# Optimization experiments

Hardware: AMD Instinct MI355X
Metric: run time of the kernel (lower is better)

Reference implementation:

```python
import jax, jax.numpy as jnp
import numpy as np

N, E, G, R = 65536, 524288, 1024, 512
D_IN, H, R_FEAT, NH, HD = 7, 128, 25, 4, 32
EPS = 1e-5


def setup_inputs() -> dict:
    key = jax.random.key(0)
    ks = jax.random.split(key, 16)
    f = lambda i, shape, s: jax.random.normal(ks[i], shape, jnp.float32) * s
    return {
        "x": jax.random.normal(ks[0], (N, D_IN), jnp.float32),
        "edge_index": jax.random.randint(ks[1], (2, E), 0, N),
        "batch": jnp.repeat(jnp.arange(G), N // G),  # 64 atoms per graph, sorted
        "per_residue_features": jax.random.normal(ks[2], (R, R_FEAT), jnp.float32),
        # GCN layer weights (PyG GCNConv: x @ W then normalized aggregation, + bias)
        "W0": f(3, (D_IN, H), 0.3), "b0": jnp.zeros(H, jnp.float32),
        "W1": f(4, (H, H), 0.1), "b1": jnp.zeros(H, jnp.float32),
        "W2": f(5, (H, H), 0.1), "b2": jnp.zeros(H, jnp.float32),
        # BatchNorm (eval mode, running stats)
        "bn_gamma": jnp.ones((3, H), jnp.float32),
        "bn_beta": jnp.zeros((3, H), jnp.float32),
        "bn_mean": f(6, (3, H), 0.1),
        "bn_var": jax.random.uniform(ks[7], (3, H), jnp.float32) + 0.5,
        # residue projection
        "res_W": f(8, (R_FEAT, H), 0.2), "res_b": jnp.zeros(H, jnp.float32),
        # MultiheadAttention packed in-proj (rows: q, k, v) and out-proj
        "in_W": f(9, (3 * H, H), 0.08), "in_b": jnp.zeros(3 * H, jnp.float32),
        "out_W": f(10, (H, H), 0.08), "out_b": jnp.zeros(H, jnp.float32),
        # classifier 128 -> 64 -> 1
        "cls_W1": f(11, (H, 64), 0.1), "cls_b1": jnp.zeros(64, jnp.float32),
        "cls_W2": f(12, (64, 1), 0.1), "cls_b2": jnp.zeros(1, jnp.float32),
    }


def reference(x, edge_index, batch, per_residue_features,
              W0, b0, W1, b1, W2, b2,
              bn_gamma, bn_beta, bn_mean, bn_var,
              res_W, res_b, in_W, in_b, out_W, out_b,
              cls_W1, cls_b1, cls_W2, cls_b2):
    src, dst = edge_index[0], edge_index[1]
    # GCN symmetric norm with self-loops: deg[i] = 1 + in-degree(i)
    deg = jnp.ones(N, x.dtype).at[dst].add(1.0)
    dinv = jax.lax.rsqrt(deg)
    enorm = (dinv[src] * dinv[dst])[:, None]      # [E,1]
    self_norm = (dinv * dinv)[:, None]            # [N,1]

    def gcn_bn_relu(h, W, b, i):
        m = h @ W                                  # [N,H]
        agg = m * self_norm
        agg = agg.at[dst].add(m[src] * enorm) + b
        y = bn_gamma[i] * (agg - bn_mean[i]) * jax.lax.rsqrt(bn_var[i] + EPS) + bn_beta[i]
        return jax.nn.relu(y)  # dropout is identity at inference

    h = gcn_bn_relu(x, W0, b0, 0)
    h = gcn_bn_relu(h, W1, b1, 1)
    h = gcn_bn_relu(h, W2, b2, 2)

    # shared residue KV (same for every graph) -> fused attention over all nodes
    res = per_residue_features @ res_W + res_b     # [R,H]
    Wq, Wk, Wv = jnp.split(in_W, 3, axis=0)
    bq, bk, bv = jnp.split(in_b, 3)
    q = (h @ Wq.T + bq).reshape(N, NH, HD)
    k = (res @ Wk.T + bk).reshape(R, NH, HD)
    v = (res @ Wv.T + bv).reshape(R, NH, HD)
    scores = jnp.einsum('nhd,rhd->nhr', q, k) / np.float32(np.sqrt(HD))
    attn = jax.nn.softmax(scores, axis=-1)         # [N,NH,R]
    o = jnp.einsum('nhr,rhd->nhd', attn, v).reshape(N, H)
    o = o @ out_W.T + out_b                        # [N,H]

    # per-graph mean pool (segment mean over batch ids)
    counts = jnp.zeros(G, o.dtype).at[batch].add(1.0)
    pooled = jnp.zeros((G, H), o.dtype).at[batch].add(o) / counts[:, None]

    hid = jax.nn.relu(pooled @ cls_W1 + cls_b1)
    logits = (hid @ cls_W2 + cls_b2)[:, 0]         # [G]
    return logits
```

## Files before the change

### kernel.cpp

```cpp
#include <hip/hip_runtime.h>
#include <math.h>

#define N_NODES 65536
#define N_EDGES 524288
#define N_GRAPHS 1024
#define H 128
#define R_RES 512
#define NH 4
#define HD 32
#define D_IN 7
#define EPS 1e-5f

typedef __attribute__((ext_vector_type(8))) short short8;
typedef __attribute__((ext_vector_type(4))) short short4v;
typedef __attribute__((ext_vector_type(4))) float f32x4;
typedef __attribute__((ext_vector_type(4))) unsigned uint4v;
typedef __attribute__((ext_vector_type(2))) unsigned uint2v;
typedef __attribute__((ext_vector_type(4))) unsigned short us4;

#if __has_builtin(__builtin_amdgcn_exp2f)
#define EXP2F __builtin_amdgcn_exp2f
#else
#define EXP2F exp2f
#endif
#if __has_builtin(__builtin_amdgcn_rcpf)
#define RCPF __builtin_amdgcn_rcpf
#else
#define RCPF(x) (1.0f/(x))
#endif

__device__ __forceinline__ f32x4 mfma_k16(short4v a, short4v b, f32x4 c){
#if defined(__HIP_DEVICE_COMPILE__)
  return __builtin_amdgcn_mfma_f32_16x16x16bf16_1k(a, b, c, 0, 0, 0);
#else
  (void)a; (void)b; return c;
#endif
}

__device__ __forceinline__ unsigned short rnd_bf16(float f){
  return (unsigned short)((__builtin_bit_cast(unsigned, f) + 0x8000u) >> 16);
}
__device__ __forceinline__ unsigned pk_bf16(float lo, float hi){
  unsigned a = __builtin_bit_cast(unsigned, lo) + 0x8000u;
  unsigned b = __builtin_bit_cast(unsigned, hi) + 0x8000u;
  return __builtin_amdgcn_perm(b, a, 0x07060302u);
}
__device__ __forceinline__ float bflo(unsigned u){ return __builtin_bit_cast(float, u << 16); }
__device__ __forceinline__ float bfhi(unsigned u){ return __builtin_bit_cast(float, u & 0xFFFF0000u); }

__device__ __forceinline__ void acc8(float* a, uint4v u, float wgt){
  a[0]=fmaf(bflo(u.x),wgt,a[0]); a[1]=fmaf(bfhi(u.x),wgt,a[1]);
  a[2]=fmaf(bflo(u.y),wgt,a[2]); a[3]=fmaf(bfhi(u.y),wgt,a[3]);
  a[4]=fmaf(bflo(u.z),wgt,a[4]); a[5]=fmaf(bfhi(u.z),wgt,a[5]);
  a[6]=fmaf(bflo(u.w),wgt,a[6]); a[7]=fmaf(bfhi(u.w),wgt,a[7]);
}

__global__ __launch_bounds__(256) void k_count(const int* __restrict__ dst, int* __restrict__ cnt, int E){
  int e = blockIdx.x*256 + threadIdx.x;
  if (e < E) atomicAdd(&cnt[dst[e]], 1);
}

__global__ __launch_bounds__(256) void k_part(const int* __restrict__ cnt, int* __restrict__ part){
  int i = blockIdx.x*256 + threadIdx.x;
  int v = cnt[i];
  #pragma unroll
  for (int off=1; off<64; off<<=1) v += __shfl_xor(v, off);
  __shared__ int red[4];
  if ((threadIdx.x & 63) == 0) red[threadIdx.x >> 6] = v;
  __syncthreads();
  if (threadIdx.x == 0) part[blockIdx.x] = red[0]+red[1]+red[2]+red[3];
}

__global__ __launch_bounds__(256) void k_scanp(int* __restrict__ part){
  __shared__ int s[256];
  int t = threadIdx.x;
  int v = part[t];
  s[t] = v;
  __syncthreads();
  for (int off=1; off<256; off<<=1){
    int u = (t >= off) ? s[t-off] : 0;
    __syncthreads();
    s[t] += u;
    __syncthreads();
  }
  part[t] = s[t] - v;
}

__global__ __launch_bounds__(256) void k_apply(const int* __restrict__ cnt, const int* __restrict__ part,
      int* __restrict__ csr_off, int* __restrict__ cursor, float* __restrict__ dinv){
  __shared__ int s[256];
  int b = blockIdx.x, t = threadIdx.x;
  int i = b*256 + t;
  int c = cnt[i];
  s[t] = c;
  __syncthreads();
  for (int off=1; off<256; off<<=1){
    int u = (t >= off) ? s[t-off] : 0;
    __syncthreads();
    s[t] += u;
    __syncthreads();
  }
  int o0 = part[b] + s[t] - c;
  csr_off[i] = o0;
  cursor[i] = o0;
  dinv[i] = rsqrtf(1.0f + (float)c);
  if (i == N_NODES-1) csr_off[N_NODES] = N_EDGES;
}

__global__ __launch_bounds__(256) void k_fill(const int* __restrict__ src, const int* __restrict__ dst,
      const float* __restrict__ dinv, int* __restrict__ cursor, int2* __restrict__ csr_ev, int E){
  int e = blockIdx.x*256 + threadIdx.x;
  if (e >= E) return;
  int s = src[e], d = dst[e];
  int p = atomicAdd(&cursor[d], 1);
  int2 rec;
  rec.x = s;
  rec.y = __builtin_bit_cast(int, dinv[s]*dinv[d]);
  csr_ev[p] = rec;
}

__global__ __launch_bounds__(256) void k_lin0(const float* __restrict__ x, const float* __restrict__ W0,
                                              unsigned short* __restrict__ out){
  int gid = blockIdx.x*256 + threadIdx.x;
  int l = threadIdx.x & 63;
  int n = __builtin_amdgcn_readfirstlane(gid >> 6);
  float a0 = 0.0f, a1 = 0.0f;
  #pragma unroll
  for (int k=0;k<D_IN;k++){
    float xv = x[(long)n*D_IN + k];
    float2 wv = *(const float2*)(W0 + k*H + 2*l);
    a0 = fmaf(xv, wv.x, a0); a1 = fmaf(xv, wv.y, a1);
  }
  *(unsigned*)(out + (long)n*H + 2*l) = pk_bf16(a0, a1);
}

__global__ __launch_bounds__(256) void k_gemm_mfma(const unsigned short* __restrict__ A,
      const float* __restrict__ Bsrc, const float* __restrict__ bias, void* __restrict__ Cout,
      int transB, int outMode){
  __shared__ unsigned short Bt[128][136];
  int tid = threadIdx.x;
  long rowBase = (long)blockIdx.x * 128;
  int w = tid >> 6, l = tid & 63;
  int lc = l & 15, q4 = l >> 4;

  if (transB){
    for (int i = tid; i < 4096; i += 256){
      int c = i >> 5, seg = i & 31;
      float4 v = *(const float4*)(Bsrc + (long)c*128 + seg*4);
      uint2 p; p.x = pk_bf16(v.x, v.y); p.y = pk_bf16(v.z, v.w);
      *(uint2*)&Bt[c][seg*4] = p;
    }
  } else {
    for (int i = tid; i < 4096; i += 256){
      int k = i >> 5, seg = i & 31;
      float4 v = *(const float4*)(Bsrc + (long)k*128 + seg*4);
      Bt[seg*4+0][k] = rnd_bf16(v.x); Bt[seg*4+1][k] = rnd_bf16(v.y);
      Bt[seg*4+2][k] = rnd_bf16(v.z); Bt[seg*4+3][k] = rnd_bf16(v.w);
    }
  }

  short8 af[2][4];
  #pragma unroll
  for (int rt=0;rt<2;rt++){
    long row = rowBase + w*32 + rt*16 + lc;
    #pragma unroll
    for (int kc=0;kc<4;kc++)
      af[rt][kc] = *(const short8*)(A + row*128 + kc*32 + q4*8);
  }

  f32x4 acc[2][8];
  #pragma unroll
  for (int rt=0;rt<2;rt++)
    #pragma unroll
    for (int ct=0;ct<8;ct++) acc[rt][ct] = (f32x4){0.f,0.f,0.f,0.f};

  __syncthreads();

  #pragma unroll
  for (int kc=0;kc<4;kc++){
    #pragma unroll
    for (int ct=0;ct<8;ct++){
      short8 bf = *(const short8*)&Bt[ct*16 + lc][kc*32 + q4*8];
      acc[0][ct] = __builtin_amdgcn_mfma_f32_16x16x32_bf16(af[0][kc], bf, acc[0][ct], 0,0,0);
      acc[1][ct] = __builtin_amdgcn_mfma_f32_16x16x32_bf16(af[1][kc], bf, acc[1][ct], 0,0,0);
    }
  }

  float bv[8];
  #pragma unroll
  for (int ct=0;ct<8;ct++) bv[ct] = bias ? bias[ct*16 + lc] : 0.0f;
  #pragma unroll
  for (int rt=0;rt<2;rt++){
    #pragma unroll
    for (int ct=0;ct<8;ct++){
      int col = ct*16 + lc;
      float vv[4];
      #pragma unroll
      for (int i=0;i<4;i++) vv[i] = acc[rt][ct][i] + bv[ct];
      long row0 = rowBase + w*32 + rt*16 + q4*4;
      if (outMode == 0){
        #pragma unroll
        for (int i=0;i<4;i++) ((unsigned short*)Cout)[(row0+i)*128 + col] = rnd_bf16(vv[i]);
      } else if (outMode == 1){
        #pragma unroll
        for (int i=0;i<4;i++) ((float*)Cout)[(row0+i)*128 + col] = vv[i];
      } else {
        us4 p = {rnd_bf16(vv[0]), rnd_bf16(vv[1]), rnd_bf16(vv[2]), rnd_bf16(vv[3])};
        *(us4*)((unsigned short*)Cout + (long)col*512 + row0) = p;
      }
    }
  }
}

__global__ __launch_bounds__(256) void k_rp(const unsigned short* __restrict__ K,
      const unsigned short* __restrict__ Vt, unsigned short* __restrict__ FK,
      unsigned short* __restrict__ FV){
  int blk = blockIdx.x;
  int t = (blk & 255)*256 + threadIdx.x;
  if (blk < 256){
    int r = t >> 7, d = t & 127;
    int h = d >> 5, q4d = (d >> 3) & 3, j = d & 7;
    int rc = r >> 4, lc = r & 15;
    FK[(((long)(h*32 + rc)*64) + q4d*16 + lc)*8 + j] = K[t];
  } else {
    int j = t & 3, half = (t >> 2) & 1, lc = (t >> 3) & 15, q4 = (t >> 7) & 3, rc = (t >> 9) & 31, h = t >> 14;
    FV[t] = Vt[(long)(h*32 + half*16 + lc)*512 + rc*16 + q4*4 + j];
  }
}

__global__ __launch_bounds__(256) void k_agg(const unsigned short* __restrict__ m, const int* __restrict__ csr_off,
      const int2* __restrict__ csr_ev, const float* __restrict__ dinv,
      const float* __restrict__ b, const float* __restrict__ gamma, const float* __restrict__ beta,
      const float* __restrict__ mean, const float* __restrict__ var, unsigned short* __restrict__ out){
  int gt = blockIdx.x*256 + threadIdx.x;
  int li = gt & 15;
  int n = gt >> 4;
  int c = li*8;
  float dn = dinv[n], sn = dn*dn;
  float a[8];
  {
    uint4v u = *(const uint4v*)(m + (long)n*H + c);
    a[0]=bflo(u.x)*sn; a[1]=bfhi(u.x)*sn; a[2]=bflo(u.y)*sn; a[3]=bfhi(u.y)*sn;
    a[4]=bflo(u.z)*sn; a[5]=bfhi(u.z)*sn; a[6]=bflo(u.w)*sn; a[7]=bfhi(u.w)*sn;
  }
  int e0 = csr_off[n], e1 = csr_off[n+1];
  int e = e0;
  for (; e + 4 <= e1; e += 4){
    int2 p0 = csr_ev[e],   p1 = csr_ev[e+1];
    int2 p2 = csr_ev[e+2], p3 = csr_ev[e+3];
    uint4v u0 = *(const uint4v*)(m + (long)p0.x*H + c);
    uint4v u1 = *(const uint4v*)(m + (long)p1.x*H + c);
    uint4v u2 = *(const uint4v*)(m + (long)p2.x*H + c);
    uint4v u3 = *(const uint4v*)(m + (long)p3.x*H + c);
    acc8(a, u0, __builtin_bit_cast(float, p0.y));
    acc8(a, u1, __builtin_bit_cast(float, p1.y));
    acc8(a, u2, __builtin_bit_cast(float, p2.y));
    acc8(a, u3, __builtin_bit_cast(float, p3.y));
  }
  for (; e < e1; e++){
    int2 p0 = csr_ev[e];
    uint4v u0 = *(const uint4v*)(m + (long)p0.x*H + c);
    acc8(a, u0, __builtin_bit_cast(float, p0.y));
  }
  float4 g0 = *(const float4*)(gamma + c), g1 = *(const float4*)(gamma + c + 4);
  float4 v0 = *(const float4*)(var   + c), v1 = *(const float4*)(var   + c + 4);
  float4 b0 = *(const float4*)(b     + c), b1 = *(const float4*)(b     + c + 4);
  float4 m0 = *(const float4*)(mean  + c), m1 = *(const float4*)(mean  + c + 4);
  float4 t0 = *(const float4*)(beta  + c), t1 = *(const float4*)(beta  + c + 4);
  float r[8];
  r[0]=fmaxf(g0.x*rsqrtf(v0.x+EPS)*(a[0]+b0.x-m0.x)+t0.x, 0.f);
  r[1]=fmaxf(g0.y*rsqrtf(v0.y+EPS)*(a[1]+b0.y-m0.y)+t0.y, 0.f);
  r[2]=fmaxf(g0.z*rsqrtf(v0.z+EPS)*(a[2]+b0.z-m0.z)+t0.z, 0.f);
  r[3]=fmaxf(g0.w*rsqrtf(v0.w+EPS)*(a[3]+b0.w-m0.w)+t0.w, 0.f);
  r[4]=fmaxf(g1.x*rsqrtf(v1.x+EPS)*(a[4]+b1.x-m1.x)+t1.x, 0.f);
  r[5]=fmaxf(g1.y*rsqrtf(v1.y+EPS)*(a[5]+b1.y-m1.y)+t1.y, 0.f);
  r[6]=fmaxf(g1.z*rsqrtf(v1.z+EPS)*(a[6]+b1.z-m1.z)+t1.z, 0.f);
  r[7]=fmaxf(g1.w*rsqrtf(v1.w+EPS)*(a[7]+b1.w-m1.w)+t1.w, 0.f);
  uint4v p;
  p.x = pk_bf16(r[0],r[1]); p.y = pk_bf16(r[2],r[3]);
  p.z = pk_bf16(r[4],r[5]); p.w = pk_bf16(r[6],r[7]);
  *(uint4v*)(out + (long)n*H + c) = p;
}

__global__ __launch_bounds__(256,2) void k_gemm(const float* __restrict__ A, const float* __restrict__ B,
      const float* __restrict__ bias, void* __restrict__ C, int K, int transB, int outBf16){
  __shared__ float Bs[128][132];
  __shared__ float As[16][128];
  int tid = threadIdx.x;
  long rowBase = (long)blockIdx.x * 128;

  if (!transB){
    for (int idx = tid; idx < 128*128; idx += 256){
      int k = idx >> 7, c = idx & 127;
      Bs[k][c] = (k < K) ? B[(long)k*128 + c] : 0.0f;
    }
  } else {
    for (int idx = tid; idx < 128*128; idx += 256){
      int c = idx >> 7, k = idx & 127;
      Bs[k][c] = (k < K) ? B[(long)c*K + k] : 0.0f;
    }
  }

  float acc[8][8];
  #pragma unroll
  for (int i=0;i<8;i++)
    #pragma unroll
    for (int j=0;j<8;j++) acc[i][j] = 0.0f;

  int rg = tid >> 4, cg = tid & 15;
  int r0 = rg*8, c0 = cg*8;
  int srow = tid >> 1, skoff = (tid & 1)*8;
  const bool fast = ((K & 15) == 0);

  for (int k0 = 0; k0 < K; k0 += 16){
    __syncthreads();
    const float* ap = A + (rowBase + srow)*K + k0 + skoff;
    if (fast){
      float4 v0 = *(const float4*)(ap);
      float4 v1 = *(const float4*)(ap + 4);
      As[skoff+0][srow] = v0.x; As[skoff+1][srow] = v0.y;
      As[skoff+2][srow] = v0.z; As[skoff+3][srow] = v0.w;
      As[skoff+4][srow] = v1.x; As[skoff+5][srow] = v1.y;
      As[skoff+6][srow] = v1.z; As[skoff+7][srow] = v1.w;
    } else {
      #pragma unroll
      for (int j=0;j<8;j++){
        int kk = k0 + skoff + j;
        As[skoff+j][srow] = (kk < K) ? ap[j] : 0.0f;
      }
    }
    __syncthreads();
    #pragma unroll
    for (int k=0;k<16;k++){
      float4 a0 = *(const float4*)(&As[k][r0]);
      float4 a1 = *(const float4*)(&As[k][r0+4]);
      float4 b0 = *(const float4*)(&Bs[k0+k][c0]);
      float4 b1 = *(const float4*)(&Bs[k0+k][c0+4]);
      float a[8] = {a0.x,a0.y,a0.z,a0.w,a1.x,a1.y,a1.z,a1.w};
      float b[8] = {b0.x,b0.y,b0.z,b0.w,b1.x,b1.y,b1.z,b1.w};
      #pragma unroll
      for (int i=0;i<8;i++)
        #pragma unroll
        for (int j=0;j<8;j++)
          acc[i][j] = fmaf(a[i], b[j], acc[i][j]);
    }
  }

  #pragma unroll
  for (int i=0;i<8;i++){
    float o[8];
    #pragma unroll
    for (int j=0;j<8;j++) o[j] = acc[i][j] + (bias ? bias[c0+j] : 0.0f);
    long row = rowBase + r0 + i;
    if (outBf16){
      uint4v p;
      p.x = pk_bf16(o[0],o[1]); p.y = pk_bf16(o[2],o[3]);
      p.z = pk_bf16(o[4],o[5]); p.w = pk_bf16(o[6],o[7]);
      *(uint4v*)((unsigned short*)C + row*128 + c0) = p;
    } else {
      float* cp = (float*)C + row*128 + c0;
      *(float4*)cp = (float4){o[0],o[1],o[2],o[3]};
      *(float4*)(cp+4) = (float4){o[4],o[5],o[6],o[7]};
    }
  }
}

__global__ __launch_bounds__(256,4) void k_attn(const unsigned short* __restrict__ hb,
      const float* __restrict__ inW, const float* __restrict__ inb,
      const unsigned short* __restrict__ Kf, const unsigned short* __restrict__ Vf,
      unsigned short* __restrict__ obuf){
  int tid = threadIdx.x;
  int h = blockIdx.y;
  int w = tid >> 6, l = tid & 63;
  int lc = l & 15, q4 = l >> 4;
  long nb = (long)blockIdx.x*256 + w*64;
  const float scale = 0.25503489f;

  int srcA = lc + (q4 & 1)*32;
  int srcB = srcA + 16;
  bool hi = (q4 >> 1) != 0;

  short8 wq[2][4];
  #pragma unroll
  for (int t=0;t<2;t++){
    #pragma unroll
    for (int kc=0;kc<4;kc++){
      const float* wp = inW + (long)(h*32 + t*16 + lc)*128 + kc*32 + q4*8;
      float4 x0 = *(const float4*)wp;
      float4 x1 = *(const float4*)(wp+4);
      uint4v p; p.x = pk_bf16(x0.x,x0.y); p.y = pk_bf16(x0.z,x0.w);
      p.z = pk_bf16(x1.x,x1.y); p.w = pk_bf16(x1.z,x1.w);
      wq[t][kc] = __builtin_bit_cast(short8, p);
    }
  }
  float bq0[4], bq1[4];
  #pragma unroll
  for (int i=0;i<4;i++){ bq0[i] = inb[h*32 + q4*4 + i]; bq1[i] = inb[h*32 + 16 + q4*4 + i]; }

  short8 qB[4];
  #pragma unroll
  for (int nt=0;nt<4;nt++){
    short8 hf[4];
    #pragma unroll
    for (int kc=0;kc<4;kc++)
      hf[kc] = *(const short8*)(hb + (nb + nt*16 + lc)*128 + kc*32 + q4*8);
    f32x4 qa0 = (f32x4){0.f,0.f,0.f,0.f};
    f32x4 qa1 = (f32x4){0.f,0.f,0.f,0.f};
    #pragma unroll
    for (int kc=0;kc<4;kc++){
      qa0 = __builtin_amdgcn_mfma_f32_16x16x32_bf16(wq[0][kc], hf[kc], qa0, 0,0,0);
      qa1 = __builtin_amdgcn_mfma_f32_16x16x32_bf16(wq[1][kc], hf[kc], qa1, 0,0,0);
    }
    unsigned P0 = pk_bf16((qa0[0]+bq0[0])*scale, (qa0[1]+bq0[1])*scale);
    unsigned P1 = pk_bf16((qa0[2]+bq0[2])*scale, (qa0[3]+bq0[3])*scale);
    unsigned P2 = pk_bf16((qa1[0]+bq1[0])*scale, (qa1[1]+bq1[1])*scale);
    unsigned P3 = pk_bf16((qa1[2]+bq1[2])*scale, (qa1[3]+bq1[3])*scale);
    unsigned x0 = __shfl(P0, srcA), x1 = __shfl(P1, srcA), x2 = __shfl(P2, srcA), x3 = __shfl(P3, srcA);
    unsigned y0 = __shfl(P0, srcB), y1 = __shfl(P1, srcB), y2 = __shfl(P2, srcB), y3 = __shfl(P3, srcB);
    uint4v bp; bp.x = hi?x2:x0; bp.y = hi?x3:x1; bp.z = hi?y2:y0; bp.w = hi?y3:y1;
    qB[nt] = __builtin_bit_cast(short8, bp);
  }

  const short4v ones4 = {(short)0x3F80,(short)0x3F80,(short)0x3F80,(short)0x3F80};
  f32x4 oA[4], oB[4], os[4];
  #pragma unroll
  for (int nt=0;nt<4;nt++){
    oA[nt] = (f32x4){0.f,0.f,0.f,0.f};
    oB[nt] = (f32x4){0.f,0.f,0.f,0.f};
    os[nt] = (f32x4){0.f,0.f,0.f,0.f};
  }

  const unsigned short* Kp = Kf + (long)h*16384 + (long)l*8;
  const unsigned short* Vp = Vf + (long)h*16384 + (long)l*8;

  for (int rc = 0; rc < 32; rc++){
    short8 kf = *(const short8*)(Kp + rc*512);
    uint4v vv = *(const uint4v*)(Vp + rc*512);
    uint2v va = {vv.x, vv.y}, vb = {vv.z, vv.w};
    short4v vfA = __builtin_bit_cast(short4v, va);
    short4v vfB = __builtin_bit_cast(short4v, vb);
    #pragma unroll
    for (int nt=0;nt<4;nt++){
      f32x4 z = {0.f,0.f,0.f,0.f};
      f32x4 s = __builtin_amdgcn_mfma_f32_16x16x32_bf16(kf, qB[nt], z, 0,0,0);
      float e0 = EXP2F(s[0]), e1 = EXP2F(s[1]), e2 = EXP2F(s[2]), e3 = EXP2F(s[3]);
      uint2v pk2; pk2.x = pk_bf16(e0, e1); pk2.y = pk_bf16(e2, e3);
      short4v pf = __builtin_bit_cast(short4v, pk2);
      oA[nt] = mfma_k16(vfA,   pf, oA[nt]);
      oB[nt] = mfma_k16(vfB,   pf, oB[nt]);
      os[nt] = mfma_k16(ones4, pf, os[nt]);
    }
  }

  #pragma unroll
  for (int nt=0;nt<4;nt++){
    float inv = RCPF(os[nt][0]);
    long node = nb + nt*16 + lc;
    us4 a = { rnd_bf16(oA[nt][0]*inv), rnd_bf16(oA[nt][1]*inv),
              rnd_bf16(oA[nt][2]*inv), rnd_bf16(oA[nt][3]*inv) };
    us4 b = { rnd_bf16(oB[nt][0]*inv), rnd_bf16(oB[nt][1]*inv),
              rnd_bf16(oB[nt][2]*inv), rnd_bf16(oB[nt][3]*inv) };
    *(us4*)(obuf + node*128 + h*32 + q4*4) = a;
    *(us4*)(obuf + node*128 + h*32 + 16 + q4*4) = b;
  }
}

__global__ __launch_bounds__(256) void k_gemm_out(const unsigned short* __restrict__ A,
      const float* __restrict__ Bsrc, const float* __restrict__ bias,
      const float* __restrict__ W1, const float* __restrict__ b1,
      const float* __restrict__ W2, const float* __restrict__ b2, float* __restrict__ out){
  __shared__ unsigned short Bt[128][136];
  __shared__ float pools[4][128];
  __shared__ float pooled[2][128];
  int tid = threadIdx.x;
  long rowBase = (long)blockIdx.x * 128;
  int w = tid >> 6, l = tid & 63;
  int lc = l & 15, q4 = l >> 4;

  for (int i = tid; i < 4096; i += 256){
    int c = i >> 5, seg = i & 31;
    float4 v = *(const float4*)(Bsrc + (long)c*128 + seg*4);
    uint2 p; p.x = pk_bf16(v.x, v.y); p.y = pk_bf16(v.z, v.w);
    *(uint2*)&Bt[c][seg*4] = p;
  }

  short8 af[2][4];
  #pragma unroll
  for (int rt=0;rt<2;rt++){
    long row = rowBase + w*32 + rt*16 + lc;
    #pragma unroll
    for (int kc=0;kc<4;kc++)
      af[rt][kc] = *(const short8*)(A + row*128 + kc*32 + q4*8);
  }

  f32x4 acc[2][8];
  #pragma unroll
  for (int rt=0;rt<2;rt++)
    #pragma unroll
    for (int ct=0;ct<8;ct++) acc[rt][ct] = (f32x4){0.f,0.f,0.f,0.f};

  __syncthreads();

  #pragma unroll
  for (int kc=0;kc<4;kc++){
    #pragma unroll
    for (int ct=0;ct<8;ct++){
      short8 bf = *(const short8*)&Bt[ct*16 + lc][kc*32 + q4*8];
      acc[0][ct] = __builtin_amdgcn_mfma_f32_16x16x32_bf16(af[0][kc], bf, acc[0][ct], 0,0,0);
      acc[1][ct] = __builtin_amdgcn_mfma_f32_16x16x32_bf16(af[1][kc], bf, acc[1][ct], 0,0,0);
    }
  }

  #pragma unroll
  for (int ct=0;ct<8;ct++){
    float ps = acc[0][ct][0]+acc[0][ct][1]+acc[0][ct][2]+acc[0][ct][3]
             + acc[1][ct][0]+acc[1][ct][1]+acc[1][ct][2]+acc[1][ct][3];
    ps += __shfl_xor(ps, 16);
    ps += __shfl_xor(ps, 32);
    if (q4 == 0) pools[w][ct*16 + lc] = ps;
  }
  __syncthreads();

  if (tid < 128){
    int c = tid;
    pooled[0][c] = (pools[0][c] + pools[1][c]) * (1.0f/64.0f) + bias[c];
    pooled[1][c] = (pools[2][c] + pools[3][c]) * (1.0f/64.0f) + bias[c];
  }
  __syncthreads();

  if (tid < 128){
    int g = tid >> 6, tp = tid & 63;
    float hh = b1[tp];
    for (int c=0;c<128;c++) hh = fmaf(pooled[g][c], W1[c*64 + tp], hh);
    hh = fmaxf(hh, 0.0f);
    float v = hh * W2[tp];
    #pragma unroll
    for (int off=32; off>0; off>>=1) v += __shfl_down(v, off);
    if (tp == 0) out[blockIdx.x*2 + g] = v + b2[0];
  }
}

extern "C" void kernel_launch(void* const* d_in, const int* in_sizes, int n_in,
                              void* d_out, int out_size, void* d_ws, size_t ws_size,
                              hipStream_t stream){
  const float* x     = (const float*)d_in[0];
  const int*   ei    = (const int*)d_in[1];
  const float* perres= (const float*)d_in[3];
  const float* W0 = (const float*)d_in[4];
  const float* b0 = (const float*)d_in[5];
  const float* W1 = (const float*)d_in[6];  const float* b1 = (const float*)d_in[7];
  const float* W2 = (const float*)d_in[8];  const float* b2 = (const float*)d_in[9];
  const float* bng = (const float*)d_in[10]; const float* bnb = (const float*)d_in[11];
  const float* bnm = (const float*)d_in[12]; const float* bnv = (const float*)d_in[13];
  const float* resW = (const float*)d_in[14]; const float* resb = (const float*)d_in[15];
  const float* inW  = (const float*)d_in[16]; const float* inb  = (const float*)d_in[17];
  const float* outW = (const float*)d_in[18]; const float* outb = (const float*)d_in[19];
  const float* cW1 = (const float*)d_in[20]; const float* cb1 = (const float*)d_in[21];
  const float* cW2 = (const float*)d_in[22]; const float* cb2 = (const float*)d_in[23];
  float* out = (float*)d_out;

  char* ws = (char*)d_ws;
  size_t off = 0;
  auto alloc = [&](size_t bytes) -> char* {
    char* p = ws + off;
    off += (bytes + 255) & ~(size_t)255;
    return p;
  };
  float* dinv    = (float*)alloc((size_t)N_NODES*4);
  int*   cnt     = (int*)  alloc((size_t)N_NODES*4);
  int*   cursor  = (int*)  alloc((size_t)N_NODES*4);
  int*   csr_off = (int*)  alloc((size_t)(N_NODES+1)*4);
  int2*  csr_ev  = (int2*) alloc((size_t)N_EDGES*8);
  int*   part    = (int*)  alloc((size_t)256*4);
  unsigned short* mb  = (unsigned short*)alloc((size_t)N_NODES*H*2);
  unsigned short* hb  = (unsigned short*)alloc((size_t)N_NODES*H*2);
  unsigned short* resbuf = (unsigned short*)alloc((size_t)R_RES*H*2);
  unsigned short* Kbf = (unsigned short*)alloc((size_t)R_RES*H*2);
  unsigned short* Vtb = (unsigned short*)alloc((size_t)H*R_RES*2);
  unsigned short* Kfr = (unsigned short*)alloc((size_t)R_RES*H*2);
  unsigned short* Vfr = (unsigned short*)alloc((size_t)H*R_RES*2);
  if (off > ws_size) return;

  const int* srcI = ei;
  const int* dstI = ei + N_EDGES;

  (void)hipMemsetAsync(cnt, 0, (size_t)N_NODES*4, stream);
  k_count<<<N_EDGES/256, 256, 0, stream>>>(dstI, cnt, N_EDGES);
  k_part <<<N_NODES/256, 256, 0, stream>>>(cnt, part);
  k_scanp<<<1, 256, 0, stream>>>(part);
  k_apply<<<N_NODES/256, 256, 0, stream>>>(cnt, part, csr_off, cursor, dinv);
  k_fill <<<N_EDGES/256, 256, 0, stream>>>(srcI, dstI, dinv, cursor, csr_ev, N_EDGES);

  const int NB = N_NODES/128;
  const int AGB = N_NODES/16;
  k_lin0<<<N_NODES/4, 256, 0, stream>>>(x, W0, mb);
  k_agg<<<AGB, 256, 0, stream>>>(mb, csr_off, csr_ev, dinv, b0, bng,     bnb,     bnm,     bnv,     hb);
  k_gemm_mfma<<<NB, 256, 0, stream>>>(hb, W1, nullptr, mb, 0, 0);
  k_agg<<<AGB, 256, 0, stream>>>(mb, csr_off, csr_ev, dinv, b1, bng+128, bnb+128, bnm+128, bnv+128, hb);
  k_gemm_mfma<<<NB, 256, 0, stream>>>(hb, W2, nullptr, mb, 0, 0);
  k_agg<<<AGB, 256, 0, stream>>>(mb, csr_off, csr_ev, dinv, b2, bng+256, bnb+256, bnm+256, bnv+256, hb);

  k_gemm<<<R_RES/128, 256, 0, stream>>>(perres, resW, resb, resbuf, 25, 0, 1);
  k_gemm_mfma<<<R_RES/128, 256, 0, stream>>>(resbuf, inW + 128*128, inb + 128, Kbf, 1, 0);
  k_gemm_mfma<<<R_RES/128, 256, 0, stream>>>(resbuf, inW + 256*128, inb + 256, Vtb, 1, 2);
  k_rp<<<512, 256, 0, stream>>>(Kbf, Vtb, Kfr, Vfr);

  dim3 agrid(N_NODES/256, NH);
  k_attn<<<agrid, 256, 0, stream>>>(hb, inW, inb, Kfr, Vfr, mb);

  k_gemm_out<<<NB, 256, 0, stream>>>(mb, outW, outb, cW1, cb1, cW2, cb2, out);
}
```

Measured before the change: 388.6 us.

## Split GCN edge gather across four lane groups and software-pipeline attention loads

The aggregation kernel now gives each node a full wavefront, splitting its edges across four 16-lane subgroups that are combined with cross-lane shuffles. Only one subgroup applies batchnorm and writes the result. This raises memory-level parallelism for the gather and evens out imbalance from varying node degrees, at the cost of four times more threads and mostly idle lanes in the epilogue. Separately, the attention loop prefetches the next K/V fragment and groups all score MFMAs ahead of the exp and accumulate stages, so load latency can overlap with compute.

After: 424.9 us. +9.4%, slower.

```diff
diff --git a/kernel.cpp b/kernel.cpp
--- a/kernel.cpp
+++ b/kernel.cpp
@@ -232,54 +232,58 @@
       const int2* __restrict__ csr_ev, const float* __restrict__ dinv,
       const float* __restrict__ b, const float* __restrict__ gamma, const float* __restrict__ beta,
       const float* __restrict__ mean, const float* __restrict__ var, unsigned short* __restrict__ out){
-  int gt = blockIdx.x*256 + threadIdx.x;
-  int li = gt & 15;
-  int n = gt >> 4;
+  int lane = threadIdx.x & 63;
+  int li = lane & 15;
+  int sg = lane >> 4;
+  int n = blockIdx.x*4 + (threadIdx.x >> 6);
   int c = li*8;
   float dn = dinv[n], sn = dn*dn;
+  float selfw = (sg == 0) ? sn : 0.0f;
   float a[8];
   {
     uint4v u = *(const uint4v*)(m + (long)n*H + c);
-    a[0]=bflo(u.x)*sn; a[1]=bfhi(u.x)*sn; a[2]=bflo(u.y)*sn; a[3]=bfhi(u.y)*sn;
-    a[4]=bflo(u.z)*sn; a[5]=bfhi(u.z)*sn; a[6]=bflo(u.w)*sn; a[7]=bfhi(u.w)*sn;
+    a[0]=bflo(u.x)*selfw; a[1]=bfhi(u.x)*selfw; a[2]=bflo(u.y)*selfw; a[3]=bfhi(u.y)*selfw;
+    a[4]=bflo(u.z)*selfw; a[5]=bfhi(u.z)*selfw; a[6]=bflo(u.w)*selfw; a[7]=bfhi(u.w)*selfw;
   }
   int e0 = csr_off[n], e1 = csr_off[n+1];
-  int e = e0;
-  for (; e + 4 <= e1; e += 4){
-    int2 p0 = csr_ev[e],   p1 = csr_ev[e+1];
-    int2 p2 = csr_ev[e+2], p3 = csr_ev[e+3];
+  int e = e0 + sg;
+  for (; e + 4 < e1; e += 8){
+    int2 p0 = csr_ev[e], p1 = csr_ev[e+4];
     uint4v u0 = *(const uint4v*)(m + (long)p0.x*H + c);
     uint4v u1 = *(const uint4v*)(m + (long)p1.x*H + c);
-    uint4v u2 = *(const uint4v*)(m + (long)p2.x*H + c);
-    uint4v u3 = *(const uint4v*)(m + (long)p3.x*H + c);
     acc8(a, u0, __builtin_bit_cast(float, p0.y));
     acc8(a, u1, __builtin_bit_cast(float, p1.y));
-    acc8(a, u2, __builtin_bit_cast(float, p2.y));
-    acc8(a, u3, __builtin_bit_cast(float, p3.y));
-  }
-  for (; e < e1; e++){
+  }
+  for (; e < e1; e += 4){
     int2 p0 = csr_ev[e];
     uint4v u0 = *(const uint4v*)(m + (long)p0.x*H + c);
     acc8(a, u0, __builtin_bit_cast(float, p0.y));
   }
-  float4 g0 = *(const float4*)(gamma + c), g1 = *(const float4*)(gamma + c + 4);
-  float4 v0 = *(const float4*)(var   + c), v1 = *(const float4*)(var   + c + 4);
-  float4 b0 = *(const float4*)(b     + c), b1 = *(const float4*)(b     + c + 4);
-  float4 m0 = *(const float4*)(mean  + c), m1 = *(const float4*)(mean  + c + 4);
-  float4 t0 = *(const float4*)(beta  + c), t1 = *(const float4*)(beta  + c + 4);
-  float r[8];
-  r[0]=fmaxf(g0.x*rsqrtf(v0.x+EPS)*(a[0]+b0.x-m0.x)+t0.x, 0.f);
-  r[1]=fmaxf(g0.y*rsqrtf(v0.y+EPS)*(a[1]+b0.y-m0.y)+t0.y, 0.f);
-  r[2]=fmaxf(g0.z*rsqrtf(v0.z+EPS)*(a[2]+b0.z-m0.z)+t0.z, 0.f);
-  r[3]=fmaxf(g0.w*rsqrtf(v0.w+EPS)*(a[3]+b0.w-m0.w)+t0.w, 0.f);
-  r[4]=fmaxf(g1.x*rsqrtf(v1.x+EPS)*(a[4]+b1.x-m1.x)+t1.x, 0.f);
-  r[5]=fmaxf(g1.y*rsqrtf(v1.y+EPS)*(a[5]+b1.y-m1.y)+t1.y, 0.f);
-  r[6]=fmaxf(g1.z*rsqrtf(v1.z+EPS)*(a[6]+b1.z-m1.z)+t1.z, 0.f);
-  r[7]=fmaxf(g1.w*rsqrtf(v1.w+EPS)*(a[7]+b1.w-m1.w)+t1.w, 0.f);
-  uint4v p;
-  p.x = pk_bf16(r[0],r[1]); p.y = pk_bf16(r[2],r[3]);
-  p.z = pk_bf16(r[4],r[5]); p.w = pk_bf16(r[6],r[7]);
-  *(uint4v*)(out + (long)n*H + c) = p;
+  #pragma unroll
+  for (int j=0;j<8;j++){
+    a[j] += __shfl_xor(a[j], 16);
+    a[j] += __shfl_xor(a[j], 32);
+  }
+  if (sg == 0){
+    float4 g0 = *(const float4*)(gamma + c), g1 = *(const float4*)(gamma + c + 4);
+    float4 v0 = *(const float4*)(var   + c), v1 = *(const float4*)(var   + c + 4);
+    float4 b0 = *(const float4*)(b     + c), b1 = *(const float4*)(b     + c + 4);
+    float4 m0 = *(const float4*)(mean  + c), m1 = *(const float4*)(mean  + c + 4);
+    float4 t0 = *(const float4*)(beta  + c), t1 = *(const float4*)(beta  + c + 4);
+    float r[8];
+    r[0]=fmaxf(g0.x*rsqrtf(v0.x+EPS)*(a[0]+b0.x-m0.x)+t0.x, 0.f);
+    r[1]=fmaxf(g0.y*rsqrtf(v0.y+EPS)*(a[1]+b0.y-m0.y)+t0.y, 0.f);
+    r[2]=fmaxf(g0.z*rsqrtf(v0.z+EPS)*(a[2]+b0.z-m0.z)+t0.z, 0.f);
+    r[3]=fmaxf(g0.w*rsqrtf(v0.w+EPS)*(a[3]+b0.w-m0.w)+t0.w, 0.f);
+    r[4]=fmaxf(g1.x*rsqrtf(v1.x+EPS)*(a[4]+b1.x-m1.x)+t1.x, 0.f);
+    r[5]=fmaxf(g1.y*rsqrtf(v1.y+EPS)*(a[5]+b1.y-m1.y)+t1.y, 0.f);
+    r[6]=fmaxf(g1.z*rsqrtf(v1.z+EPS)*(a[6]+b1.z-m1.z)+t1.z, 0.f);
+    r[7]=fmaxf(g1.w*rsqrtf(v1.w+EPS)*(a[7]+b1.w-m1.w)+t1.w, 0.f);
+    uint4v p;
+    p.x = pk_bf16(r[0],r[1]); p.y = pk_bf16(r[2],r[3]);
+    p.z = pk_bf16(r[4],r[5]); p.w = pk_bf16(r[6],r[7]);
+    *(uint4v*)(out + (long)n*H + c) = p;
+  }
 }
 
 __global__ __launch_bounds__(256,2) void k_gemm(const float* __restrict__ A, const float* __restrict__ B,
@@ -433,23 +437,36 @@
   const unsigned short* Kp = Kf + (long)h*16384 + (long)l*8;
   const unsigned short* Vp = Vf + (long)h*16384 + (long)l*8;
 
+  short8 kf = *(const short8*)(Kp);
+  uint4v vv = *(const uint4v*)(Vp);
   for (int rc = 0; rc < 32; rc++){
-    short8 kf = *(const short8*)(Kp + rc*512);
-    uint4v vv = *(const uint4v*)(Vp + rc*512);
+    int rcn = (rc < 31) ? rc+1 : 31;
+    short8 kfn = *(const short8*)(Kp + rcn*512);
+    uint4v vvn = *(const uint4v*)(Vp + rcn*512);
     uint2v va = {vv.x, vv.y}, vb = {vv.z, vv.w};
     short4v vfA = __builtin_bit_cast(short4v, va);
     short4v vfB = __builtin_bit_cast(short4v, vb);
+    f32x4 s[4];
     #pragma unroll
     for (int nt=0;nt<4;nt++){
       f32x4 z = {0.f,0.f,0.f,0.f};
-      f32x4 s = __builtin_amdgcn_mfma_f32_16x16x32_bf16(kf, qB[nt], z, 0,0,0);
-      float e0 = EXP2F(s[0]), e1 = EXP2F(s[1]), e2 = EXP2F(s[2]), e3 = EXP2F(s[3]);
+      s[nt] = __builtin_amdgcn_mfma_f32_16x16x32_bf16(kf, qB[nt], z, 0,0,0);
+    }
+    short4v pf[4];
+    #pragma unroll
+    for (int nt=0;nt<4;nt++){
+      float e0 = EXP2F(s[nt][0]), e1 = EXP2F(s[nt][1]);
+      float e2 = EXP2F(s[nt][2]), e3 = EXP2F(s[nt][3]);
       uint2v pk2; pk2.x = pk_bf16(e0, e1); pk2.y = pk_bf16(e2, e3);
-      short4v pf = __builtin_bit_cast(short4v, pk2);
-      oA[nt] = mfma_k16(vfA,   pf, oA[nt]);
-      oB[nt] = mfma_k16(vfB,   pf, oB[nt]);
-      os[nt] = mfma_k16(ones4, pf, os[nt]);
-    }
+      pf[nt] = __builtin_bit_cast(short4v, pk2);
+    }
+    #pragma unroll
+    for (int nt=0;nt<4;nt++){
+      oA[nt] = mfma_k16(vfA,   pf[nt], oA[nt]);
+      oB[nt] = mfma_k16(vfB,   pf[nt], oB[nt]);
+      os[nt] = mfma_k16(ones4, pf[nt], os[nt]);
+    }
+    kf = kfn; vv = vvn;
   }
 
   #pragma unroll
@@ -592,7 +609,7 @@
   k_fill <<<N_EDGES/256, 256, 0, stream>>>(srcI, dstI, dinv, cursor, csr_ev, N_EDGES);
 
   const int NB = N_NODES/128;
-  const int AGB = N_NODES/16;
+  const int AGB = N_NODES/4;
   k_lin0<<<N_NODES/4, 256, 0, stream>>>(x, W0, mb);
   k_agg<<<AGB, 256, 0, stream>>>(mb, csr_off, csr_ev, dinv, b0, bng,     bnb,     bnm,     bnv,     hb);
   k_gemm_mfma<<<NB, 256, 0, stream>>>(hb, W1, nullptr, mb, 0, 0);
```
